# Kernel tuning notes

Measured on AMD Instinct MI355X. Metric: run time of the kernel, lower is better.

The kernel has to match this reference:

```python
import jax, jax.numpy as jnp
import numpy as np

N = 12000      # nodes
E = 384000     # edges (avg degree 32)
IN, HID, OUT = 128, 128, 40
BETA, ITERS = 0.5, 25   # Bjorck order-2 projection params (module defaults)


def setup_inputs() -> dict:
    key = jax.random.key(0)
    ks = jax.random.split(key, 6)
    x = jax.random.normal(ks[0], (N, IN), jnp.float32)
    edge_index = jax.random.randint(ks[1], (2, E), 0, N, dtype=jnp.int32)
    W1 = jax.random.normal(ks[2], (HID, IN), jnp.float32)
    W2 = jax.random.normal(ks[3], (HID, HID), jnp.float32)
    lin_w = jax.random.normal(ks[4], (OUT, HID), jnp.float32) / np.float32(np.sqrt(HID))
    lin_b = jax.random.normal(ks[5], (OUT,), jnp.float32) * 0.01
    return {"x": x, "W1": W1, "W2": W2, "lin_w": lin_w, "lin_b": lin_b,
            "edge_index": edge_index}


def _bjorck(w):
    # order-2 Bjorck orthonormalization (beta fixed at 0.5):
    # w <- 15/8 w - 5/4 w(w^T w) + 3/8 w(w^T w)^2
    for _ in range(ITERS):
        wtw = w.T @ w
        w = 1.875 * w - 1.25 * (w @ wtw) + 0.375 * (w @ (wtw @ wtw))
    return w


def _orthonormal(W):
    # scale_values: sqrt(||W||_inf * ||W||_1) upper-bounds the spectral norm
    # (computed on .data in torch -> stop_gradient here)
    scaling = jnp.sqrt(jnp.abs(W).sum(axis=1).max() * jnp.abs(W).sum(axis=0).max())
    scaling = jax.lax.stop_gradient(scaling)
    return _bjorck(W.T / scaling).T  # [out, in]


def _normalized_adj(edge_index):
    # to_dense_adj (scatter-add) then D^{-1/2} A^T D^{-1/2} exactly as
    # normalize_tensor_adj: adj.dot(D^{-1/2}).T.dot(D^{-1/2})
    r, c = edge_index[0], edge_index[1]
    adj = jnp.zeros((N, N), jnp.float32).at[r, c].add(1.0)
    rowsum = adj.sum(axis=1)
    d = jnp.where(rowsum > 0, rowsum ** -0.5, 0.0)
    return d[:, None] * adj.T * d[None, :]


def reference(x, W1, W2, lin_w, lin_b, edge_index):
    norm_adj = _normalized_adj(edge_index)          # [N, N]
    h = jax.nn.relu(norm_adj @ (x @ _orthonormal(W1).T))   # [N, HID]
    h = jax.nn.relu(norm_adj @ (h @ _orthonormal(W2).T))   # [N, HID]
    # dropout inactive (eval mode)
    logits = h @ lin_w.T + lin_b                    # [N, OUT]
    return jax.nn.log_softmax(logits, axis=1)
```

## Files before the change

### kernel.cpp

```cpp
#include <hip/hip_runtime.h>
#include <math.h>

#define NN 12000
#define EE 384000
#define FF 128
#define NOUT 40
#define BJ_MAX 25
#define NWARM 8
#define EXIT_TOL 3e-3f

typedef __attribute__((ext_vector_type(8))) short bf16x8;
typedef __attribute__((ext_vector_type(4))) short s16x4;
typedef __attribute__((ext_vector_type(4))) float f32x4;
typedef unsigned short ushort_t;

__device__ __forceinline__ ushort_t f2bf(float x) {
  unsigned u = __float_as_uint(x);
  unsigned r = (u + 0x7FFFu + ((u >> 16) & 1u)) >> 16;
  return (ushort_t)r;
}
__device__ __forceinline__ float bf2f(ushort_t h) {
  return __uint_as_float(((unsigned)h) << 16);
}
__device__ __forceinline__ int swz(int r, int c) {
  return ((r << 8) + (c << 1)) ^ ((r & 7) << 4);
}

__global__ __launch_bounds__(256) void build_deg(const int* __restrict__ ei,
    float* __restrict__ degf, int* __restrict__ cnt) {
  int e = blockIdx.x * 256 + threadIdx.x;
  if (e >= EE) return;
  atomicAdd(&degf[ei[e]], 1.0f);
  atomicAdd(&cnt[ei[EE + e]], 1);
}

__global__ __launch_bounds__(1024) void scan_dinv_kernel(const int* __restrict__ cnt,
    int* __restrict__ rowstart, const float* __restrict__ degf, float* __restrict__ dinv) {
  __shared__ int sums[1024];
  int tid = threadIdx.x;
  const int CH = 12;
  int base = tid * CH;
  int local[CH];
  int s = 0;
  #pragma unroll
  for (int m = 0; m < CH; m++) {
    int idx = base + m;
    int v = (idx < NN) ? cnt[idx] : 0;
    local[m] = s;
    s += v;
  }
  sums[tid] = s;
  __syncthreads();
  for (int off = 1; off < 1024; off <<= 1) {
    int v = (tid >= off) ? sums[tid - off] : 0;
    __syncthreads();
    sums[tid] += v;
    __syncthreads();
  }
  int excl = (tid > 0) ? sums[tid - 1] : 0;
  #pragma unroll
  for (int m = 0; m < CH; m++) {
    int idx = base + m;
    if (idx < NN) rowstart[idx] = excl + local[m];
  }
  if (tid == 1023) rowstart[NN] = sums[1023];
  for (int i = tid; i < NN; i += 1024) {
    float dv = degf[i];
    dinv[i] = (dv > 0.0f) ? (1.0f / sqrtf(dv)) : 0.0f;
  }
}

__global__ __launch_bounds__(256) void scatter_edges(const int* __restrict__ ei,
    const int* __restrict__ rowstart, int* __restrict__ fill, int* __restrict__ srcl) {
  int e = blockIdx.x * 256 + threadIdx.x;
  if (e >= EE) return;
  int r = ei[e], c = ei[EE + e];
  int pos = rowstart[c] + atomicAdd(&fill[c], 1);
  srcl[pos] = r;
}

__device__ __forceinline__ void mm_product(const char* Xh, const char* Xl,
    const char* Yh, const char* Yl, int R0, int C0, int lane, f32x4 (&acc)[2][4]) {
  int rl = lane & 15;
  int kq = (lane >> 4) * 8;
  #pragma unroll
  for (int k0 = 0; k0 < 128; k0 += 32) {
    bf16x8 ah[2], al[2];
    #pragma unroll
    for (int i = 0; i < 2; i++) {
      ah[i] = *(const bf16x8*)(Xh + swz(R0 + i * 16 + rl, k0 + kq));
      al[i] = *(const bf16x8*)(Xl + swz(R0 + i * 16 + rl, k0 + kq));
    }
    #pragma unroll
    for (int j = 0; j < 4; j++) {
      bf16x8 bh = *(const bf16x8*)(Yh + swz(C0 + j * 16 + rl, k0 + kq));
      bf16x8 bl = *(const bf16x8*)(Yl + swz(C0 + j * 16 + rl, k0 + kq));
      #pragma unroll
      for (int i = 0; i < 2; i++) {
        acc[i][j] = __builtin_amdgcn_mfma_f32_16x16x32_bf16(ah[i], bh, acc[i][j], 0, 0, 0);
        acc[i][j] = __builtin_amdgcn_mfma_f32_16x16x32_bf16(ah[i], bl, acc[i][j], 0, 0, 0);
        acc[i][j] = __builtin_amdgcn_mfma_f32_16x16x32_bf16(al[i], bh, acc[i][j], 0, 0, 0);
      }
    }
  }
}

__device__ __forceinline__ void store_C(char* Ch, char* Cl, int R0, int C0,
    int lane, f32x4 (&acc)[2][4]) {
  int cl = lane & 15, rq = (lane >> 4) * 4;
  #pragma unroll
  for (int i = 0; i < 2; i++)
  #pragma unroll
  for (int j = 0; j < 4; j++) {
    int col = C0 + j * 16 + cl;
    int row = R0 + i * 16 + rq;
    s16x4 hv, lv;
    #pragma unroll
    for (int t = 0; t < 4; t++) {
      float x = acc[i][j][t];
      ushort_t h = f2bf(x);
      ushort_t lo = f2bf(x - bf2f(h));
      hv[t] = (short)h; lv[t] = (short)lo;
    }
    *(s16x4*)(Ch + swz(col, row)) = hv;
    *(s16x4*)(Cl + swz(col, row)) = lv;
  }
}

__device__ __forceinline__ void store_CR(char* Ch, char* Cl, char* Rh, char* Rl,
    int R0, int C0, int lane, f32x4 (&acc)[2][4]) {
  int cl = lane & 15, rq = (lane >> 4) * 4;
  #pragma unroll
  for (int i = 0; i < 2; i++)
  #pragma unroll
  for (int j = 0; j < 4; j++) {
    int col = C0 + j * 16 + cl;
    int row = R0 + i * 16 + rq;
    s16x4 hv, lv;
    #pragma unroll
    for (int t = 0; t < 4; t++) {
      float x = acc[i][j][t];
      ushort_t h = f2bf(x);
      ushort_t lo = f2bf(x - bf2f(h));
      hv[t] = (short)h; lv[t] = (short)lo;
    }
    *(s16x4*)(Ch + swz(col, row)) = hv;
    *(s16x4*)(Cl + swz(col, row)) = lv;
    #pragma unroll
    for (int t = 0; t < 4; t++) {
      *(ushort_t*)(Rh + swz(row + t, col)) = (ushort_t)(unsigned short)hv[t];
      *(ushort_t*)(Rl + swz(row + t, col)) = (ushort_t)(unsigned short)lv[t];
    }
  }
}

__global__ __launch_bounds__(512) void bjorck_mfma(const float* __restrict__ W1,
    const float* __restrict__ W2, ushort_t* __restrict__ wfc) {
  __shared__ char lds[131072];
  __shared__ float wmax[8];
  char* P0h = lds;
  char* P0l = lds + 32768;
  char* P1h = lds + 65536;
  char* P1l = lds + 98304;
  const int L = blockIdx.x;
  const float* Wsrc = (L == 0) ? W1 : W2;
  int tid = threadIdx.x;
  int lane = tid & 63;
  int wv = tid >> 6;
  int R0 = (wv >> 1) * 32;
  int C0 = (wv & 1) * 64;

  float* f = (float*)lds;
  if (tid < 256) {
    float s = 0.0f;
    if (tid < 128) {
      for (int j = 0; j < FF; j++) s += fabsf(Wsrc[tid * FF + j]);
    } else {
      int c = tid - 128;
      for (int j = 0; j < FF; j++) s += fabsf(Wsrc[j * FF + c]);
    }
    f[tid] = s;
  }
  __syncthreads();
  if (tid == 0) {
    float rm = 0.0f, cm = 0.0f;
    for (int i = 0; i < 128; i++) { rm = fmaxf(rm, f[i]); cm = fmaxf(cm, f[128 + i]); }
    f[256] = 1.0f / sqrtf(rm * cm);
  }
  __syncthreads();
  float inv_s = f[256];
  __syncthreads();

  {
    int r = tid >> 2, c0 = (tid & 3) * 32;
    #pragma unroll
    for (int mm = 0; mm < 32; mm += 8) {
      bf16x8 hv, lv;
      #pragma unroll
      for (int t = 0; t < 8; t++) {
        float x = Wsrc[r * FF + c0 + mm + t] * inv_s;
        ushort_t h = f2bf(x);
        ushort_t lo = f2bf(x - bf2f(h));
        hv[t] = (short)h; lv[t] = (short)lo;
      }
      *(bf16x8*)(P0h + swz(r, c0 + mm)) = hv;
      *(bf16x8*)(P0l + swz(r, c0 + mm)) = lv;
      #pragma unroll
      for (int t = 0; t < 8; t++) {
        *(ushort_t*)(P1h + swz(c0 + mm + t, r)) = (ushort_t)(unsigned short)hv[t];
        *(ushort_t*)(P1l + swz(c0 + mm + t, r)) = (ushort_t)(unsigned short)lv[t];
      }
    }
  }
  __syncthreads();

  for (int it = 0; it < BJ_MAX; it++) {
    float ca, cb, cc;
    if (it < NWARM)       { ca = 3.4445f; cb = -4.7750f; cc = 2.0315f; }
    else if (it == NWARM) { ca = 2.1479f; cb = -1.7258f; cc = 0.5645f; }
    else                  { ca = 1.875f;  cb = -1.25f;   cc = 0.375f; }

    f32x4 m_acc[2][4] = {};
    mm_product(P0h, P0l, P0h, P0l, R0, C0, lane, m_acc);

    {
      int cl = lane & 15, rq = (lane >> 4) * 4;
      float lmax = 0.0f;
      #pragma unroll
      for (int i = 0; i < 2; i++)
      #pragma unroll
      for (int j = 0; j < 4; j++)
      #pragma unroll
      for (int t = 0; t < 4; t++) {
        int row = R0 + i * 16 + rq + t;
        int col = C0 + j * 16 + cl;
        float d = m_acc[i][j][t] - ((row == col) ? 1.0f : 0.0f);
        lmax = fmaxf(lmax, fabsf(d));
      }
      #pragma unroll
      for (int off = 32; off; off >>= 1) lmax = fmaxf(lmax, __shfl_xor(lmax, off));
      if (lane == 0) wmax[wv] = lmax;
    }
    __syncthreads();
    {
      float gmax = 0.0f;
      #pragma unroll
      for (int w = 0; w < 8; w++) gmax = fmaxf(gmax, wmax[w]);
      if (gmax < EXIT_TOL) break;
    }
    store_C(P0h, P0l, R0, C0, lane, m_acc);
    __syncthreads();

    f32x4 p_acc[2][4] = {};
    mm_product(P0h, P0l, P0h, P0l, R0, C0, lane, p_acc);
    {
      int cl = lane & 15, rq = (lane >> 4) * 4;
      #pragma unroll
      for (int i = 0; i < 2; i++)
      #pragma unroll
      for (int j = 0; j < 4; j++)
      #pragma unroll
      for (int t = 0; t < 4; t++) {
        int row = R0 + i * 16 + rq + t;
        int col = C0 + j * 16 + cl;
        float pv = cb * m_acc[i][j][t] + cc * p_acc[i][j][t];
        if (row == col) pv += ca;
        p_acc[i][j][t] = pv;
      }
    }
    __syncthreads();
    store_C(P0h, P0l, R0, C0, lane, p_acc);
    __syncthreads();

    f32x4 v_acc[2][4] = {};
    mm_product(P0h, P0l, P1h, P1l, R0, C0, lane, v_acc);
    __syncthreads();
    store_CR(P1h, P1l, P0h, P0l, R0, C0, lane, v_acc);
    __syncthreads();
  }

  {
    ushort_t* oh = wfc + L * 32768;
    ushort_t* ol = oh + 16384;
    int r = tid >> 2;
    int q = tid & 3;
    #pragma unroll
    for (int b = 0; b < 4; b++) {
      int c0 = q * 32 + b * 8;
      bf16x8 hv = *(const bf16x8*)(P0h + swz(r, c0));
      bf16x8 lv = *(const bf16x8*)(P0l + swz(r, c0));
      *(bf16x8*)(oh + r * FF + c0) = hv;
      *(bf16x8*)(ol + r * FF + c0) = lv;
    }
  }
}

__global__ __launch_bounds__(256) void gemm_mfma(const float* __restrict__ X,
    const ushort_t* __restrict__ wc, float* __restrict__ Out) {
  __shared__ char xlds[32768];
  char* Xh = xlds;
  char* Xl = xlds + 16384;
  int tid = threadIdx.x;
  int row0 = blockIdx.x * 64;

  {
    int r = tid >> 2;
    int q = (tid & 3) * 32;
    int gr = row0 + r;
    #pragma unroll
    for (int b = 0; b < 32; b += 8) {
      bf16x8 hv, lv;
      if (gr < NN) {
        const float4* xp4 = (const float4*)(X + gr * FF + q + b);
        float4 v0 = xp4[0];
        float4 v1 = xp4[1];
        float xv[8] = {v0.x, v0.y, v0.z, v0.w, v1.x, v1.y, v1.z, v1.w};
        #pragma unroll
        for (int t = 0; t < 8; t++) {
          ushort_t h = f2bf(xv[t]);
          hv[t] = (short)h;
          lv[t] = (short)f2bf(xv[t] - bf2f(h));
        }
      } else {
        #pragma unroll
        for (int t = 0; t < 8; t++) { hv[t] = 0; lv[t] = 0; }
      }
      *(bf16x8*)(Xh + swz(r, q + b)) = hv;
      *(bf16x8*)(Xl + swz(r, q + b)) = lv;
    }
  }
  __syncthreads();

  int lane = tid & 63, wv = tid >> 6;
  int R0 = (wv & 1) * 32;
  int C0 = (wv >> 1) * 64;
  int rl = lane & 15, kq = (lane >> 4) * 8;
  f32x4 acc[2][4] = {};
  #pragma unroll
  for (int k0 = 0; k0 < 128; k0 += 32) {
    bf16x8 ah[2], al[2];
    #pragma unroll
    for (int i = 0; i < 2; i++) {
      ah[i] = *(const bf16x8*)(Xh + swz(R0 + i * 16 + rl, k0 + kq));
      al[i] = *(const bf16x8*)(Xl + swz(R0 + i * 16 + rl, k0 + kq));
    }
    #pragma unroll
    for (int j = 0; j < 4; j++) {
      const ushort_t* bp = wc + (C0 + j * 16 + rl) * FF + k0 + kq;
      bf16x8 bh = *(const bf16x8*)bp;
      bf16x8 bl = *(const bf16x8*)(bp + 16384);
      #pragma unroll
      for (int i = 0; i < 2; i++) {
        acc[i][j] = __builtin_amdgcn_mfma_f32_16x16x32_bf16(ah[i], bh, acc[i][j], 0, 0, 0);
        acc[i][j] = __builtin_amdgcn_mfma_f32_16x16x32_bf16(ah[i], bl, acc[i][j], 0, 0, 0);
        acc[i][j] = __builtin_amdgcn_mfma_f32_16x16x32_bf16(al[i], bh, acc[i][j], 0, 0, 0);
      }
    }
  }
  int rq = (lane >> 4) * 4;
  #pragma unroll
  for (int i = 0; i < 2; i++)
  #pragma unroll
  for (int j = 0; j < 4; j++) {
    int col = C0 + j * 16 + rl;
    #pragma unroll
    for (int t = 0; t < 4; t++) {
      int node = row0 + R0 + i * 16 + rq + t;
      if (node < NN) Out[node * FF + col] = acc[i][j][t];
    }
  }
}

__global__ __launch_bounds__(256) void spmm_relu(const float* __restrict__ G,
    float* __restrict__ Hout, const float* __restrict__ dinv,
    const int* __restrict__ rowstart, const int* __restrict__ srcl) {
  int g = threadIdx.x >> 5;
  int lane = threadIdx.x & 31;
  int row = blockIdx.x * 8 + g;
  int s = rowstart[row], e = rowstart[row + 1];
  const float4* G4 = (const float4*)G;
  float4 acc = make_float4(0.f, 0.f, 0.f, 0.f);
  for (int p = s; p < e; p++) {
    int r = srcl[p];
    float dr = dinv[r];
    float4 gv = G4[r * 32 + lane];
    acc.x += dr * gv.x; acc.y += dr * gv.y; acc.z += dr * gv.z; acc.w += dr * gv.w;
  }
  float dc = dinv[row];
  float4 o;
  o.x = fmaxf(dc * acc.x, 0.f); o.y = fmaxf(dc * acc.y, 0.f);
  o.z = fmaxf(dc * acc.z, 0.f); o.w = fmaxf(dc * acc.w, 0.f);
  ((float4*)Hout)[row * 32 + lane] = o;
}

__global__ __launch_bounds__(256) void spmm_head(const float* __restrict__ G,
    const float* __restrict__ dinv, const int* __restrict__ rowstart,
    const int* __restrict__ srcl, const float* __restrict__ lw,
    const float* __restrict__ lb, float* __restrict__ out) {
  __shared__ float slw[NOUT * 130];
  __shared__ float slb[64];
  __shared__ float sh[8][128];
  int tid = threadIdx.x;
  for (int i = tid; i < NOUT * 128; i += 256) {
    int r = i >> 7, c = i & 127;
    slw[r * 130 + c] = lw[r * FF + c];
  }
  if (tid < 64) slb[tid] = (tid < NOUT) ? lb[tid] : 0.0f;

  {
    int g = tid >> 5, lane32 = tid & 31;
    int row = blockIdx.x * 8 + g;
    int s = rowstart[row], e = rowstart[row + 1];
    const float4* G4 = (const float4*)G;
    float4 acc = make_float4(0.f, 0.f, 0.f, 0.f);
    for (int p = s; p < e; p++) {
      int r = srcl[p];
      float dr = dinv[r];
      float4 gv = G4[r * 32 + lane32];
      acc.x += dr * gv.x; acc.y += dr * gv.y; acc.z += dr * gv.z; acc.w += dr * gv.w;
    }
    float dc = dinv[row];
    float4 o;
    o.x = fmaxf(dc * acc.x, 0.f); o.y = fmaxf(dc * acc.y, 0.f);
    o.z = fmaxf(dc * acc.z, 0.f); o.w = fmaxf(dc * acc.w, 0.f);
    ((float4*)&sh[g][0])[lane32] = o;
  }
  __syncthreads();

  int lane = tid & 63, w = tid >> 6;
  int ll = (lane < NOUT) ? lane : 0;
  const float2* wrow = (const float2*)(slw + ll * 130);
  #pragma unroll
  for (int rr = 0; rr < 2; rr++) {
    int lrow = w * 2 + rr;
    int node = blockIdx.x * 8 + lrow;
    const float2* hrow = (const float2*)&sh[lrow][0];
    float val = slb[lane];
    #pragma unroll 4
    for (int k = 0; k < 64; k++) {
      float2 w2 = wrow[k];
      float2 h2 = hrow[k];
      val += w2.x * h2.x + w2.y * h2.y;
    }
    float m = (lane < NOUT) ? val : -INFINITY;
    for (int off = 32; off; off >>= 1) m = fmaxf(m, __shfl_down(m, off));
    m = __shfl(m, 0);
    float ex = (lane < NOUT) ? expf(val - m) : 0.0f;
    float ssum = ex;
    for (int off = 32; off; off >>= 1) ssum += __shfl_down(ssum, off);
    ssum = __shfl(ssum, 0);
    if (lane < NOUT) out[node * NOUT + lane] = val - m - logf(ssum);
  }
}

extern "C" void kernel_launch(void* const* d_in, const int* in_sizes, int n_in,
                              void* d_out, int out_size, void* d_ws, size_t ws_size,
                              hipStream_t stream) {
  const float* x  = (const float*)d_in[0];
  const float* W1 = (const float*)d_in[1];
  const float* W2 = (const float*)d_in[2];
  const float* lw = (const float*)d_in[3];
  const float* lb = (const float*)d_in[4];
  const int*   ei = (const int*)d_in[5];
  float* out = (float*)d_out;

  float* base = (float*)d_ws;
  float* wf   = base;
  float* degf = wf + 32768;
  int* cnt      = (int*)(degf + NN);
  int* fill     = cnt + NN;
  float* dinv = (float*)(fill + NN);
  int* rowstart = (int*)(dinv + NN);
  int* srcl     = rowstart + 12004;
  float* bufA = (float*)(srcl + EE);
  float* bufB = bufA + NN * FF;
  ushort_t* wfc = (ushort_t*)wf;

  (void)hipMemsetAsync(degf, 0, 3 * NN * sizeof(float), stream);

  build_deg<<<(EE + 255) / 256, 256, 0, stream>>>(ei, degf, cnt);
  scan_dinv_kernel<<<1, 1024, 0, stream>>>(cnt, rowstart, degf, dinv);
  scatter_edges<<<(EE + 255) / 256, 256, 0, stream>>>(ei, rowstart, fill, srcl);
  bjorck_mfma<<<2, 512, 0, stream>>>(W1, W2, wfc);

  gemm_mfma<<<(NN + 63) / 64, 256, 0, stream>>>(x, wfc, bufA);
  spmm_relu<<<NN / 8, 256, 0, stream>>>(bufA, bufB, dinv, rowstart, srcl);
  gemm_mfma<<<(NN + 63) / 64, 256, 0, stream>>>(bufB, wfc + 32768, bufA);
  spmm_head<<<NN / 8, 256, 0, stream>>>(bufA, dinv, rowstart, srcl, lw, lb, out);
}
```

Baseline: 288.6 us.

## Co-schedule degree build with Bjorck and edge scatter with first GEMM

```diff
diff --git a/kernel.cpp b/kernel.cpp
--- a/kernel.cpp
+++ b/kernel.cpp
@@ -8,6 +8,7 @@
 #define BJ_MAX 25
 #define NWARM 8
 #define EXIT_TOL 3e-3f
+#define GEMM_BLOCKS ((NN + 63) / 64)
 
 typedef __attribute__((ext_vector_type(8))) short bf16x8;
 typedef __attribute__((ext_vector_type(4))) short s16x4;
@@ -24,14 +25,6 @@
 }
 __device__ __forceinline__ int swz(int r, int c) {
   return ((r << 8) + (c << 1)) ^ ((r & 7) << 4);
-}
-
-__global__ __launch_bounds__(256) void build_deg(const int* __restrict__ ei,
-    float* __restrict__ degf, int* __restrict__ cnt) {
-  int e = blockIdx.x * 256 + threadIdx.x;
-  if (e >= EE) return;
-  atomicAdd(&degf[ei[e]], 1.0f);
-  atomicAdd(&cnt[ei[EE + e]], 1);
 }
 
 __global__ __launch_bounds__(1024) void scan_dinv_kernel(const int* __restrict__ cnt,
@@ -70,15 +63,6 @@
   }
 }
 
-__global__ __launch_bounds__(256) void scatter_edges(const int* __restrict__ ei,
-    const int* __restrict__ rowstart, int* __restrict__ fill, int* __restrict__ srcl) {
-  int e = blockIdx.x * 256 + threadIdx.x;
-  if (e >= EE) return;
-  int r = ei[e], c = ei[EE + e];
-  int pos = rowstart[c] + atomicAdd(&fill[c], 1);
-  srcl[pos] = r;
-}
-
 __device__ __forceinline__ void mm_product(const char* Xh, const char* Xl,
     const char* Yh, const char* Yl, int R0, int C0, int lane, f32x4 (&acc)[2][4]) {
   int rl = lane & 15;
@@ -154,8 +138,19 @@
   }
 }
 
-__global__ __launch_bounds__(512) void bjorck_mfma(const float* __restrict__ W1,
-    const float* __restrict__ W2, ushort_t* __restrict__ wfc) {
+__global__ __launch_bounds__(512) void bjorck_deg(const int* __restrict__ ei,
+    float* __restrict__ degf, int* __restrict__ cnt,
+    const float* __restrict__ W1, const float* __restrict__ W2,
+    ushort_t* __restrict__ wfc) {
+  if (blockIdx.x >= 2) {
+    int e = (blockIdx.x - 2) * 512 + threadIdx.x;
+    if (e < EE) {
+      atomicAdd(&degf[ei[e]], 1.0f);
+      atomicAdd(&cnt[ei[EE + e]], 1);
+    }
+    return;
+  }
+
   __shared__ char lds[131072];
   __shared__ float wmax[8];
   char* P0h = lds;
@@ -223,7 +218,7 @@
     f32x4 m_acc[2][4] = {};
     mm_product(P0h, P0l, P0h, P0l, R0, C0, lane, m_acc);
 
-    {
+    if (it > NWARM) {
       int cl = lane & 15, rq = (lane >> 4) * 4;
       float lmax = 0.0f;
       #pragma unroll
@@ -240,13 +235,13 @@
       #pragma unroll
       for (int off = 32; off; off >>= 1) lmax = fmaxf(lmax, __shfl_xor(lmax, off));
       if (lane == 0) wmax[wv] = lmax;
-    }
-    __syncthreads();
-    {
+      __syncthreads();
       float gmax = 0.0f;
       #pragma unroll
       for (int w = 0; w < 8; w++) gmax = fmaxf(gmax, wmax[w]);
       if (gmax < EXIT_TOL) break;
+    } else {
+      __syncthreads();
     }
     store_C(P0h, P0l, R0, C0, lane, m_acc);
     __syncthreads();
@@ -295,8 +290,20 @@
   }
 }
 
-__global__ __launch_bounds__(256) void gemm_mfma(const float* __restrict__ X,
-    const ushort_t* __restrict__ wc, float* __restrict__ Out) {
+__global__ __launch_bounds__(256) void scatter_gemm1(const int* __restrict__ ei,
+    const int* __restrict__ rowstart, int* __restrict__ fill, int* __restrict__ srcl,
+    const float* __restrict__ X, const ushort_t* __restrict__ wc,
+    float* __restrict__ Out) {
+  if (blockIdx.x >= GEMM_BLOCKS) {
+    int e = (blockIdx.x - GEMM_BLOCKS) * 256 + threadIdx.x;
+    if (e < EE) {
+      int r = ei[e], c = ei[EE + e];
+      int pos = rowstart[c] + atomicAdd(&fill[c], 1);
+      srcl[pos] = r;
+    }
+    return;
+  }
+
   __shared__ char xlds[32768];
   char* Xh = xlds;
   char* Xl = xlds + 16384;
@@ -371,6 +378,82 @@
   }
 }
 
+__global__ __launch_bounds__(256) void gemm_mfma(const float* __restrict__ X,
+    const ushort_t* __restrict__ wc, float* __restrict__ Out) {
+  __shared__ char xlds[32768];
+  char* Xh = xlds;
+  char* Xl = xlds + 16384;
+  int tid = threadIdx.x;
+  int row0 = blockIdx.x * 64;
+
+  {
+    int r = tid >> 2;
+    int q = (tid & 3) * 32;
+    int gr = row0 + r;
+    #pragma unroll
+    for (int b = 0; b < 32; b += 8) {
+      bf16x8 hv, lv;
+      if (gr < NN) {
+        const float4* xp4 = (const float4*)(X + gr * FF + q + b);
+        float4 v0 = xp4[0];
+        float4 v1 = xp4[1];
+        float xv[8] = {v0.x, v0.y, v0.z, v0.w, v1.x, v1.y, v1.z, v1.w};
+        #pragma unroll
+        for (int t = 0; t < 8; t++) {
+          ushort_t h = f2bf(xv[t]);
+          hv[t] = (short)h;
+          lv[t] = (short)f2bf(xv[t] - bf2f(h));
+        }
+      } else {
+        #pragma unroll
+        for (int t = 0; t < 8; t++) { hv[t] = 0; lv[t] = 0; }
+      }
+      *(bf16x8*)(Xh + swz(r, q + b)) = hv;
+      *(bf16x8*)(Xl + swz(r, q + b)) = lv;
+    }
+  }
+  __syncthreads();
+
+  int lane = tid & 63, wv = tid >> 6;
+  int R0 = (wv & 1) * 32;
+  int C0 = (wv >> 1) * 64;
+  int rl = lane & 15, kq = (lane >> 4) * 8;
+  f32x4 acc[2][4] = {};
+  #pragma unroll
+  for (int k0 = 0; k0 < 128; k0 += 32) {
+    bf16x8 ah[2], al[2];
+    #pragma unroll
+    for (int i = 0; i < 2; i++) {
+      ah[i] = *(const bf16x8*)(Xh + swz(R0 + i * 16 + rl, k0 + kq));
+      al[i] = *(const bf16x8*)(Xl + swz(R0 + i * 16 + rl, k0 + kq));
+    }
+    #pragma unroll
+    for (int j = 0; j < 4; j++) {
+      const ushort_t* bp = wc + (C0 + j * 16 + rl) * FF + k0 + kq;
+      bf16x8 bh = *(const bf16x8*)bp;
+      bf16x8 bl = *(const bf16x8*)(bp + 16384);
+      #pragma unroll
+      for (int i = 0; i < 2; i++) {
+        acc[i][j] = __builtin_amdgcn_mfma_f32_16x16x32_bf16(ah[i], bh, acc[i][j], 0, 0, 0);
+        acc[i][j] = __builtin_amdgcn_mfma_f32_16x16x32_bf16(ah[i], bl, acc[i][j], 0, 0, 0);
+        acc[i][j] = __builtin_amdgcn_mfma_f32_16x16x32_bf16(al[i], bh, acc[i][j], 0, 0, 0);
+      }
+    }
+  }
+  int rq = (lane >> 4) * 4;
+  #pragma unroll
+  for (int i = 0; i < 2; i++)
+  #pragma unroll
+  for (int j = 0; j < 4; j++) {
+    int col = C0 + j * 16 + rl;
+    #pragma unroll
+    for (int t = 0; t < 4; t++) {
+      int node = row0 + R0 + i * 16 + rq + t;
+      if (node < NN) Out[node * FF + col] = acc[i][j][t];
+    }
+  }
+}
+
 __global__ __launch_bounds__(256) void spmm_relu(const float* __restrict__ G,
     float* __restrict__ Hout, const float* __restrict__ dinv,
     const int* __restrict__ rowstart, const int* __restrict__ srcl) {
@@ -379,17 +462,27 @@
   int row = blockIdx.x * 8 + g;
   int s = rowstart[row], e = rowstart[row + 1];
   const float4* G4 = (const float4*)G;
-  float4 acc = make_float4(0.f, 0.f, 0.f, 0.f);
-  for (int p = s; p < e; p++) {
-    int r = srcl[p];
-    float dr = dinv[r];
-    float4 gv = G4[r * 32 + lane];
-    acc.x += dr * gv.x; acc.y += dr * gv.y; acc.z += dr * gv.z; acc.w += dr * gv.w;
+  float4 a0 = make_float4(0.f, 0.f, 0.f, 0.f);
+  float4 a1 = make_float4(0.f, 0.f, 0.f, 0.f);
+  int p = s;
+  for (; p + 2 <= e; p += 2) {
+    int r0 = srcl[p], r1 = srcl[p + 1];
+    float d0 = dinv[r0], d1 = dinv[r1];
+    float4 g0 = G4[r0 * 32 + lane];
+    float4 g1 = G4[r1 * 32 + lane];
+    a0.x += d0 * g0.x; a0.y += d0 * g0.y; a0.z += d0 * g0.z; a0.w += d0 * g0.w;
+    a1.x += d1 * g1.x; a1.y += d1 * g1.y; a1.z += d1 * g1.z; a1.w += d1 * g1.w;
+  }
+  if (p < e) {
+    int r0 = srcl[p];
+    float d0 = dinv[r0];
+    float4 g0 = G4[r0 * 32 + lane];
+    a0.x += d0 * g0.x; a0.y += d0 * g0.y; a0.z += d0 * g0.z; a0.w += d0 * g0.w;
   }
   float dc = dinv[row];
   float4 o;
-  o.x = fmaxf(dc * acc.x, 0.f); o.y = fmaxf(dc * acc.y, 0.f);
-  o.z = fmaxf(dc * acc.z, 0.f); o.w = fmaxf(dc * acc.w, 0.f);
+  o.x = fmaxf(dc * (a0.x + a1.x), 0.f); o.y = fmaxf(dc * (a0.y + a1.y), 0.f);
+  o.z = fmaxf(dc * (a0.z + a1.z), 0.f); o.w = fmaxf(dc * (a0.w + a1.w), 0.f);
   ((float4*)Hout)[row * 32 + lane] = o;
 }
 
@@ -401,9 +494,11 @@
   __shared__ float slb[64];
   __shared__ float sh[8][128];
   int tid = threadIdx.x;
-  for (int i = tid; i < NOUT * 128; i += 256) {
-    int r = i >> 7, c = i & 127;
-    slw[r * 130 + c] = lw[r * FF + c];
+  for (int i = tid; i < NOUT * 32; i += 256) {
+    int r = i >> 5, c4 = i & 31;
+    float4 v = ((const float4*)lw)[r * 32 + c4];
+    float* dst = slw + r * 130 + c4 * 4;
+    dst[0] = v.x; dst[1] = v.y; dst[2] = v.z; dst[3] = v.w;
   }
   if (tid < 64) slb[tid] = (tid < NOUT) ? lb[tid] : 0.0f;
 
@@ -412,17 +507,27 @@
     int row = blockIdx.x * 8 + g;
     int s = rowstart[row], e = rowstart[row + 1];
     const float4* G4 = (const float4*)G;
-    float4 acc = make_float4(0.f, 0.f, 0.f, 0.f);
-    for (int p = s; p < e; p++) {
-      int r = srcl[p];
-      float dr = dinv[r];
-      float4 gv = G4[r * 32 + lane32];
-      acc.x += dr * gv.x; acc.y += dr * gv.y; acc.z += dr * gv.z; acc.w += dr * gv.w;
+    float4 a0 = make_float4(0.f, 0.f, 0.f, 0.f);
+    float4 a1 = make_float4(0.f, 0.f, 0.f, 0.f);
+    int p = s;
+    for (; p + 2 <= e; p += 2) {
+      int r0 = srcl[p], r1 = srcl[p + 1];
+      float d0 = dinv[r0], d1 = dinv[r1];
+      float4 g0 = G4[r0 * 32 + lane32];
+      float4 g1 = G4[r1 * 32 + lane32];
+      a0.x += d0 * g0.x; a0.y += d0 * g0.y; a0.z += d0 * g0.z; a0.w += d0 * g0.w;
+      a1.x += d1 * g1.x; a1.y += d1 * g1.y; a1.z += d1 * g1.z; a1.w += d1 * g1.w;
+    }
+    if (p < e) {
+      int r0 = srcl[p];
+      float d0 = dinv[r0];
+      float4 g0 = G4[r0 * 32 + lane32];
+      a0.x += d0 * g0.x; a0.y += d0 * g0.y; a0.z += d0 * g0.z; a0.w += d0 * g0.w;
     }
     float dc = dinv[row];
     float4 o;
-    o.x = fmaxf(dc * acc.x, 0.f); o.y = fmaxf(dc * acc.y, 0.f);
-    o.z = fmaxf(dc * acc.z, 0.f); o.w = fmaxf(dc * acc.w, 0.f);
+    o.x = fmaxf(dc * (a0.x + a1.x), 0.f); o.y = fmaxf(dc * (a0.y + a1.y), 0.f);
+    o.z = fmaxf(dc * (a0.z + a1.z), 0.f); o.w = fmaxf(dc * (a0.w + a1.w), 0.f);
     ((float4*)&sh[g][0])[lane32] = o;
   }
   __syncthreads();
@@ -478,12 +583,10 @@
 
   (void)hipMemsetAsync(degf, 0, 3 * NN * sizeof(float), stream);
 
-  build_deg<<<(EE + 255) / 256, 256, 0, stream>>>(ei, degf, cnt);
+  bjorck_deg<<<2 + (EE + 511) / 512, 512, 0, stream>>>(ei, degf, cnt, W1, W2, wfc);
   scan_dinv_kernel<<<1, 1024, 0, stream>>>(cnt, rowstart, degf, dinv);
-  scatter_edges<<<(EE + 255) / 256, 256, 0, stream>>>(ei, rowstart, fill, srcl);
-  bjorck_mfma<<<2, 512, 0, stream>>>(W1, W2, wfc);
-
-  gemm_mfma<<<(NN + 63) / 64, 256, 0, stream>>>(x, wfc, bufA);
+  scatter_gemm1<<<GEMM_BLOCKS + (EE + 255) / 256, 256, 0, stream>>>(
+      ei, rowstart, fill, srcl, x, wfc, bufA);
   spmm_relu<<<NN / 8, 256, 0, stream>>>(bufA, bufB, dinv, rowstart, srcl);
   gemm_mfma<<<(NN + 63) / 64, 256, 0, stream>>>(bufB, wfc + 32768, bufA);
   spmm_head<<<NN / 8, 256, 0, stream>>>(bufA, dinv, rowstart, srcl, lw, lb, out);
```

After: 235.0 us. 18.6% less time.
